# Kernel tuning notes

Hardware: AMD Instinct MI355X
Metric: run time of the kernel (lower is better)

## Reference

```python
import jax, jax.numpy as jnp
import numpy as np

TWO_PI = 2.0 * np.pi
HID, FREQ, OUT = 64, 10, 16
BS, T, K, D = 1024, 128, 8, 32
IN_DIM = K * D


def hard_sigmoid(x):
    # torch.nn.Hardsigmoid: clip(x/6 + 1/2, 0, 1)
    return jnp.clip(x / 6.0 + 0.5, 0.0, 1.0)


def setup_inputs() -> dict:
    key = jax.random.key(0)
    ks = jax.random.split(key, 16)
    s_in = 1.0 / np.sqrt(IN_DIM)
    s_h = 1.0 / np.sqrt(HID)
    inp = {
        "g1": jax.random.normal(ks[0], (BS, T, K, D), jnp.float32),
        "W_i": jax.random.normal(ks[1], (IN_DIM, HID), jnp.float32) * s_in,
        "U_i": jax.random.normal(ks[2], (HID, HID), jnp.float32) * s_h,
        "b_i": jnp.zeros((HID,), jnp.float32),
        "W_ste": jax.random.normal(ks[3], (IN_DIM, HID), jnp.float32) * s_in,
        "U_ste": jax.random.normal(ks[4], (HID, HID), jnp.float32) * s_h,
        "b_ste": jnp.ones((HID,), jnp.float32),
        "W_fre": jax.random.normal(ks[5], (IN_DIM, FREQ), jnp.float32) * s_in,
        "U_fre": jax.random.normal(ks[6], (HID, FREQ), jnp.float32) * s_h,
        "b_fre": jnp.ones((FREQ,), jnp.float32),
        "W_c": jax.random.normal(ks[7], (IN_DIM, HID), jnp.float32) * s_in,
        "U_c": jax.random.normal(ks[8], (HID, HID), jnp.float32) * s_h,
        "b_c": jnp.zeros((HID,), jnp.float32),
        "W_o": jax.random.normal(ks[9], (IN_DIM, HID), jnp.float32) * s_in,
        "U_o": jax.random.normal(ks[10], (HID, HID), jnp.float32) * s_h,
        "b_o": jnp.zeros((HID,), jnp.float32),
        "U_a": jax.random.normal(ks[11], (FREQ, 1), jnp.float32) / np.sqrt(FREQ),
        "b_a": jnp.zeros((HID,), jnp.float32),
        "W_p": jax.random.normal(ks[12], (HID, OUT), jnp.float32) * s_h,
        "b_p": jnp.zeros((OUT,), jnp.float32),
        "fc_w": jax.random.normal(ks[13], (OUT, 1), jnp.float32) / np.sqrt(OUT),
        "fc_b": jnp.zeros((1,), jnp.float32),
    }
    return inp


def reference(g1, W_i, U_i, b_i, W_ste, U_ste, b_ste, W_fre, U_fre, b_fre,
              W_c, U_c, b_c, W_o, U_o, b_o, U_a, b_a, W_p, b_p, fc_w, fc_b):
    bs, Tn, k, d = g1.shape
    x_seq = g1.reshape(bs, Tn, k * d).transpose(1, 0, 2)  # (T, bs, IN)
    H, F = U_i.shape[0], U_fre.shape[1]
    freq = jnp.arange(F, dtype=g1.dtype) / F                 # frequency vector
    h0 = jnp.zeros((bs, H), g1.dtype)
    S0 = jnp.zeros((bs, H, F), g1.dtype)
    times = jnp.arange(1, Tn + 1, dtype=g1.dtype)            # time = t+1 per step

    def step(carry, inp):
        h, S_re, S_im = carry
        x, t = inp
        i = hard_sigmoid(x @ W_i + b_i + h @ U_i)
        ste = hard_sigmoid(x @ W_ste + b_ste + h @ U_ste)    # (bs,H)
        fre = hard_sigmoid(x @ W_fre + b_fre + h @ U_fre)    # (bs,F)
        f = ste[:, :, None] * fre[:, None, :]                # (bs,H,F)
        c = i * jnp.tanh(x @ W_c + b_c + h @ U_c)            # (bs,H)
        omega = TWO_PI * t * freq                            # (F,)
        S_re = f * S_re + c[:, :, None] * jnp.cos(omega)
        S_im = f * S_im + c[:, :, None] * jnp.sin(omega)
        A = S_re * S_re + S_im * S_im                        # (bs,H,F)
        a = jnp.tanh(jnp.einsum('bhf,f->bh', A, U_a[:, 0]) + b_a)
        o = hard_sigmoid(x @ W_o + b_o + h @ U_o)
        return (o * a, S_re, S_im), None

    (hT, _, _), _ = jax.lax.scan(step, (h0, S0, S0), (x_seq, times))
    p = hT @ W_p + b_p                                       # (bs, OUT)
    return p @ fc_w + fc_b                                   # pred: (bs, 1)
```

## Files before the change

kernel.cpp:

```cpp
#include <hip/hip_runtime.h>
#include <cstdint>

#define TSTEPS  128
#define INDIM   256
#define HIDDEN  64
#define FREQN   10
#define NOUT    16
#define XSTRIDE 272
#define NTILE   17

typedef __attribute__((ext_vector_type(8))) short bf16x8;
typedef __attribute__((ext_vector_type(4))) float f32x4;

__device__ __forceinline__ unsigned short bf16h(float x) {
    unsigned u = __float_as_uint(x);
    return (unsigned short)((u + 0x7FFFu + ((u >> 16) & 1u)) >> 16);
}
__device__ __forceinline__ float rdlane(float v, int l) {
    return __int_as_float(__builtin_amdgcn_readlane(__float_as_int(v), l));
}
__device__ __forceinline__ float hsig(float x) {
    return fminf(fmaxf(__fmaf_rn(x, (1.0f / 6.0f), 0.5f), 0.0f), 1.0f);
}
__device__ __forceinline__ float tanh_f(float x) {
    float e = __expf(2.0f * x);
    return 1.0f - 2.0f / (e + 1.0f);
}

__global__ void pack_w(const float* __restrict__ Wi, const float* __restrict__ Wst,
                       const float* __restrict__ Wc, const float* __restrict__ Wo,
                       const float* __restrict__ Wfr,
                       const float* __restrict__ bi, const float* __restrict__ bst,
                       const float* __restrict__ bc, const float* __restrict__ bo,
                       const float* __restrict__ bfr,
                       unsigned short* __restrict__ Wpk, float* __restrict__ bias)
{
    int idx = blockIdx.x * 256 + threadIdx.x;
    if (idx < 8 * NTILE * 64) {
        int l = idx & 63;
        int t = (idx >> 6) % NTILE;
        int s = idx / (64 * NTILE);
        int n = t * 16 + (l & 15);
        unsigned short* dst = Wpk + (size_t)idx * 16;
        #pragma unroll
        for (int i = 0; i < 8; ++i) {
            int k = s * 32 + (l >> 4) * 8 + i;
            float v;
            if      (n < 64)  v = Wi [k * 64 + n];
            else if (n < 128) v = Wst[k * 64 + (n - 64)];
            else if (n < 192) v = Wc [k * 64 + (n - 128)];
            else if (n < 256) v = Wo [k * 64 + (n - 192)];
            else if (n < 266) v = Wfr[k * 10 + (n - 256)];
            else              v = 0.f;
            unsigned short h = bf16h(v);
            float hf = __uint_as_float((unsigned)h << 16);
            dst[i]     = h;
            dst[8 + i] = bf16h(v - hf);
        }
    } else if (idx < 8 * NTILE * 64 + XSTRIDE) {
        int n = idx - 8 * NTILE * 64;
        float b;
        if      (n < 64)  b = bi [n];
        else if (n < 128) b = bst[n - 64];
        else if (n < 192) b = bc [n - 128];
        else if (n < 256) b = bo [n - 192];
        else if (n < 266) b = bfr[n - 256];
        else              b = 0.f;
        bias[n] = b;
    }
}

__global__ __launch_bounds__(256, 2)
void gemm_mfma(const float* __restrict__ A, const unsigned short* __restrict__ Wpk,
               const float* __restrict__ bias, float* __restrict__ outp,
               int ci, int tclog)
{
    const int tid = threadIdx.x;
    const int w   = tid >> 6, l = tid & 63;
    const int l15 = l & 15,  lg = l >> 4;
    const int tcm = (1 << tclog) - 1;
    const int rbase = blockIdx.x * 128 + w * 32;

    f32x4 acc[2][NTILE];
    #pragma unroll
    for (int rt = 0; rt < 2; ++rt)
        #pragma unroll
        for (int t = 0; t < NTILE; ++t) acc[rt][t] = (f32x4){0.f, 0.f, 0.f, 0.f};

    #pragma unroll
    for (int s = 0; s < 8; ++s) {
        bf16x8 ahi[2], alo[2];
        #pragma unroll
        for (int rt = 0; rt < 2; ++rt) {
            int rp   = rbase + rt * 16 + l15;
            int grow = ((rp >> tclog) << 7) + (ci << tclog) + (rp & tcm);
            const float* ap = A + (size_t)grow * INDIM + s * 32 + lg * 8;
            float4 a0 = *reinterpret_cast<const float4*>(ap);
            float4 a1 = *reinterpret_cast<const float4*>(ap + 4);
            float av[8] = {a0.x, a0.y, a0.z, a0.w, a1.x, a1.y, a1.z, a1.w};
            union { bf16x8 v; unsigned short u[8]; } H, L;
            #pragma unroll
            for (int i = 0; i < 8; ++i) {
                unsigned short h = bf16h(av[i]);
                H.u[i] = h;
                L.u[i] = bf16h(av[i] - __uint_as_float((unsigned)h << 16));
            }
            ahi[rt] = H.v; alo[rt] = L.v;
        }
        #pragma unroll
        for (int t = 0; t < NTILE; ++t) {
            const bf16x8* bp =
                reinterpret_cast<const bf16x8*>(Wpk + ((size_t)(s * NTILE + t) * 64 + l) * 16);
            bf16x8 bhi = bp[0], blo = bp[1];
            #pragma unroll
            for (int rt = 0; rt < 2; ++rt) {
                acc[rt][t] = __builtin_amdgcn_mfma_f32_16x16x32_bf16(ahi[rt], bhi, acc[rt][t], 0, 0, 0);
                acc[rt][t] = __builtin_amdgcn_mfma_f32_16x16x32_bf16(ahi[rt], blo, acc[rt][t], 0, 0, 0);
                acc[rt][t] = __builtin_amdgcn_mfma_f32_16x16x32_bf16(alo[rt], bhi, acc[rt][t], 0, 0, 0);
            }
        }
    }
    #pragma unroll
    for (int t = 0; t < NTILE; ++t) {
        float bv = bias[t * 16 + l15];
        #pragma unroll
        for (int rt = 0; rt < 2; ++rt) {
            int rp0 = rbase + rt * 16 + lg * 4;
            #pragma unroll
            for (int r = 0; r < 4; ++r)
                outp[(size_t)(rp0 + r) * XSTRIDE + t * 16 + l15] = acc[rt][t][r] + bv;
        }
    }
}

__global__ void cstab_kernel(float2* __restrict__ tab)
{
    int idx = blockIdx.x * 256 + threadIdx.x;
    if (idx >= TSTEPS * FREQN) return;
    int t = idx / FREQN, j = idx - t * FREQN;
    float time = (float)(t + 1);
    float om = (6.28318530717958647692f * time) * ((float)j / 10.0f);
    float s, c;
    sincosf(om, &s, &c);
    tab[idx] = make_float2(c, s);
}

__global__ __launch_bounds__(256, 3)
void rec_kernel(const float* __restrict__ xproj,
                const float* __restrict__ Ui, const float* __restrict__ Us,
                const float* __restrict__ Uc, const float* __restrict__ Uo,
                const float* __restrict__ Ufre, const float* __restrict__ Ua,
                const float* __restrict__ ba,
                const float2* __restrict__ csTab,
                float* __restrict__ state,
                const float* __restrict__ Wp, const float* __restrict__ bp,
                const float* __restrict__ fcw, const float* __restrict__ fcb,
                float* __restrict__ outv,
                int ci, int TC, int nchunks)
{
    __shared__ f32x4 pg[4][64];
    __shared__ float pf_[4][16];
    __shared__ float hlds[64];
    const int tid  = threadIdx.x;
    const int lane = tid & 63, w = tid >> 6;
    const int row  = blockIdx.x;
    const int k0   = w * 16;
    const int jc   = (lane < FREQN) ? lane : (FREQN - 1);

    float4 Ur[16]; float Uf[16];
    #pragma unroll
    for (int i = 0; i < 16; ++i) {
        int k = k0 + i;
        Ur[i] = make_float4(Ui[k * 64 + lane], Us[k * 64 + lane],
                            Uc[k * 64 + lane], Uo[k * 64 + lane]);
        Uf[i] = Ufre[k * FREQN + jc];
    }

    float hv;
    float Sre[FREQN], Sim[FREQN];
    if (ci == 0) {
        hv = 0.f;
        #pragma unroll
        for (int j = 0; j < FREQN; ++j) { Sre[j] = 0.f; Sim[j] = 0.f; }
    } else {
        hv = state[row * 64 + lane];
        if (w == 0) {
            #pragma unroll
            for (int j = 0; j < FREQN; ++j) {
                Sre[j] = state[65536 + j * 65536 + row * 64 + lane];
                Sim[j] = state[65536 + 655360 + j * 65536 + row * 64 + lane];
            }
        }
    }

    const float ba_l = ba[lane];
    float sua[FREQN];
    #pragma unroll
    for (int j = 0; j < FREQN; ++j) sua[j] = Ua[j];

    const float* xb = xproj + (size_t)row * TC * XSTRIDE;
    float xi = 0.f, xs = 0.f, xc = 0.f, xo = 0.f, xf = 0.f;
    float2 cv = make_float2(0.f, 0.f);
    if (w == 0) {
        xi = xb[lane]; xs = xb[64 + lane]; xc = xb[128 + lane];
        xo = xb[192 + lane]; xf = xb[256 + jc];
        cv = csTab[(ci * TC) * FREQN + jc];
    }

    for (int tt = 0; tt < TC; ++tt) {
        float ai = 0.f, as_ = 0.f, ac = 0.f, ao = 0.f, af = 0.f;
        #pragma unroll
        for (int i = 0; i < 16; ++i) {
            float hk = rdlane(hv, k0 + i);
            ai  = __fmaf_rn(hk, Ur[i].x, ai);
            as_ = __fmaf_rn(hk, Ur[i].y, as_);
            ac  = __fmaf_rn(hk, Ur[i].z, ac);
            ao  = __fmaf_rn(hk, Ur[i].w, ao);
            af  = __fmaf_rn(hk, Uf[i],  af);
        }
        pg[w][lane] = (f32x4){ai, as_, ac, ao};
        if (lane < FREQN) pf_[w][lane] = af;
        __syncthreads();

        if (w == 0) {
            f32x4 q0 = pg[0][lane], q1 = pg[1][lane], q2 = pg[2][lane], q3 = pg[3][lane];
            float si = (q0[0] + q1[0]) + (q2[0] + q3[0]);
            float ss = (q0[1] + q1[1]) + (q2[1] + q3[1]);
            float sc = (q0[2] + q1[2]) + (q2[2] + q3[2]);
            float so = (q0[3] + q1[3]) + (q2[3] + q3[3]);
            float pfr = (pf_[0][jc] + pf_[1][jc]) + (pf_[2][jc] + pf_[3][jc]);
            float cxi = xi, cxs = xs, cxc = xc, cxo = xo, cxf = xf;
            float2 ccv = cv;
            if (tt + 1 < TC) {
                const float* b2 = xb + (size_t)(tt + 1) * XSTRIDE;
                xi = b2[lane]; xs = b2[64 + lane]; xc = b2[128 + lane];
                xo = b2[192 + lane]; xf = b2[256 + jc];
                cv = csTab[(ci * TC + tt + 1) * FREQN + jc];
            }
            float gi = hsig(cxi + si);
            float gs = hsig(cxs + ss);
            float go = hsig(cxo + so);
            float gc = gi * tanh_f(cxc + sc);
            float pfull = cxf + pfr;
            float aacc = 0.f;
            #pragma unroll
            for (int j = 0; j < FREQN; ++j) {
                float fre = hsig(rdlane(pfull, j));
                float cj = rdlane(ccv.x, j);
                float sj = rdlane(ccv.y, j);
                float fj = gs * fre;
                Sre[j] = __fmaf_rn(fj, Sre[j], gc * cj);
                Sim[j] = __fmaf_rn(fj, Sim[j], gc * sj);
                float Aj = __fmaf_rn(Sre[j], Sre[j], Sim[j] * Sim[j]);
                aacc = __fmaf_rn(Aj, sua[j], aacc);
            }
            hlds[lane] = go * tanh_f(aacc + ba_l);
        }
        __syncthreads();
        hv = hlds[lane];
    }

    if (ci == nchunks - 1) {
        if (w == 0) {
            float wef = 0.f;
            #pragma unroll
            for (int o = 0; o < NOUT; ++o)
                wef = __fmaf_rn(Wp[lane * NOUT + o], fcw[o], wef);
            float v = hv * wef;
            #pragma unroll
            for (int off = 32; off > 0; off >>= 1) v += __shfl_xor(v, off, 64);
            if (lane == 0) {
                float cb = fcb[0];
                #pragma unroll
                for (int o = 0; o < NOUT; ++o) cb = __fmaf_rn(bp[o], fcw[o], cb);
                outv[row] = v + cb;
            }
        }
    } else if (w == 0) {
        state[row * 64 + lane] = hv;
        #pragma unroll
        for (int j = 0; j < FREQN; ++j) {
            state[65536 + j * 65536 + row * 64 + lane] = Sre[j];
            state[65536 + 655360 + j * 65536 + row * 64 + lane] = Sim[j];
        }
    }
}

extern "C" void kernel_launch(void* const* d_in, const int* in_sizes, int n_in,
                              void* d_out, int out_size, void* d_ws, size_t ws_size,
                              hipStream_t stream)
{
    const float* g1  = (const float*)d_in[0];
    const float* Wi  = (const float*)d_in[1];
    const float* Ui  = (const float*)d_in[2];
    const float* bi  = (const float*)d_in[3];
    const float* Wst = (const float*)d_in[4];
    const float* Ust = (const float*)d_in[5];
    const float* bst = (const float*)d_in[6];
    const float* Wfr = (const float*)d_in[7];
    const float* Ufq = (const float*)d_in[8];
    const float* bfr = (const float*)d_in[9];
    const float* Wc  = (const float*)d_in[10];
    const float* Uc  = (const float*)d_in[11];
    const float* bc  = (const float*)d_in[12];
    const float* Wo  = (const float*)d_in[13];
    const float* Uo  = (const float*)d_in[14];
    const float* bo  = (const float*)d_in[15];
    const float* Ua  = (const float*)d_in[16];
    const float* ba  = (const float*)d_in[17];
    const float* Wp  = (const float*)d_in[18];
    const float* bp  = (const float*)d_in[19];
    const float* fcw = (const float*)d_in[20];
    const float* fcb = (const float*)d_in[21];
    float* outv = (float*)d_out;

    const size_t stateFloats = 65536 + 2 * 655360;
    const size_t csFloats    = TSTEPS * FREQN * 2;
    const size_t wpkShorts   = (size_t)8 * NTILE * 64 * 16;
    int TC = 128;
    while (TC > 8 &&
           ((size_t)1024 * TC * XSTRIDE + stateFloats + csFloats + XSTRIDE) * 4
               + wpkShorts * 2 > ws_size)
        TC >>= 1;
    int tclog = 31 - __builtin_clz((unsigned)TC);
    int nchunks = TSTEPS / TC;

    float*  xproj = (float*)d_ws;
    float*  state = xproj + (size_t)1024 * TC * XSTRIDE;
    float2* csTab = (float2*)(state + stateFloats);
    float*  bias  = (float*)(csTab + TSTEPS * FREQN);
    unsigned short* Wpk = (unsigned short*)(bias + XSTRIDE);

    pack_w<<<36, 256, 0, stream>>>(Wi, Wst, Wc, Wo, Wfr, bi, bst, bc, bo, bfr, Wpk, bias);
    cstab_kernel<<<(TSTEPS * FREQN + 255) / 256, 256, 0, stream>>>(csTab);

    const int Mt = (1024 * TC) / 128;
    for (int ci = 0; ci < nchunks; ++ci) {
        gemm_mfma<<<Mt, 256, 0, stream>>>(g1, Wpk, bias, xproj, ci, tclog);
        rec_kernel<<<1024, 256, 0, stream>>>(xproj, Ui, Ust, Uc, Uo, Ufq, Ua, ba,
                                             csTab, state, Wp, bp, fcw, fcb, outv,
                                             ci, TC, nchunks);
    }
}
```

Before: 554.1 us.

## Process two batch rows per 512-thread block in the recurrent kernel

The recurrent kernel now launches 512-thread blocks, each handling two batch rows, so 512 blocks run instead of 1024. Each of the 8 waves keeps 8 rows of the U matrices in registers and computes partial products for both rows, and two waves then run the gate and state update in parallel instead of one. The sin/cos table is read as scalar loads rather than broadcast with readlane, and hard-sigmoid on the frequency gate is applied before the broadcast. The aim is to spread the serial per-step work across more waves and reuse the U registers for two rows, at the cost of larger reductions through shared memory and fewer blocks.

```diff
diff --git a/kernel.cpp b/kernel.cpp
--- a/kernel.cpp
+++ b/kernel.cpp
@@ -145,50 +145,52 @@
     tab[idx] = make_float2(c, s);
 }
 
-__global__ __launch_bounds__(256, 3)
+__global__ __launch_bounds__(512, 2)
 void rec_kernel(const float* __restrict__ xproj,
                 const float* __restrict__ Ui, const float* __restrict__ Us,
                 const float* __restrict__ Uc, const float* __restrict__ Uo,
                 const float* __restrict__ Ufre, const float* __restrict__ Ua,
                 const float* __restrict__ ba,
-                const float2* __restrict__ csTab,
+                const float* __restrict__ csTab,
                 float* __restrict__ state,
                 const float* __restrict__ Wp, const float* __restrict__ bp,
                 const float* __restrict__ fcw, const float* __restrict__ fcb,
                 float* __restrict__ outv,
                 int ci, int TC, int nchunks)
 {
-    __shared__ f32x4 pg[4][64];
-    __shared__ float pf_[4][16];
-    __shared__ float hlds[64];
+    __shared__ f32x4 pg[2][8][64];
+    __shared__ float pf_[2][8][16];
+    __shared__ float hlds[2][64];
     const int tid  = threadIdx.x;
     const int lane = tid & 63, w = tid >> 6;
-    const int row  = blockIdx.x;
-    const int k0   = w * 16;
+    const int row0 = blockIdx.x * 2;
+    const int myrow = row0 + w;
+    const int k0   = w * 8;
     const int jc   = (lane < FREQN) ? lane : (FREQN - 1);
 
-    float4 Ur[16]; float Uf[16];
-    #pragma unroll
-    for (int i = 0; i < 16; ++i) {
+    float4 Ur[8]; float Uf[8];
+    #pragma unroll
+    for (int i = 0; i < 8; ++i) {
         int k = k0 + i;
         Ur[i] = make_float4(Ui[k * 64 + lane], Us[k * 64 + lane],
                             Uc[k * 64 + lane], Uo[k * 64 + lane]);
         Uf[i] = Ufre[k * FREQN + jc];
     }
 
-    float hv;
+    float hv0, hv1;
     float Sre[FREQN], Sim[FREQN];
     if (ci == 0) {
-        hv = 0.f;
+        hv0 = 0.f; hv1 = 0.f;
         #pragma unroll
         for (int j = 0; j < FREQN; ++j) { Sre[j] = 0.f; Sim[j] = 0.f; }
     } else {
-        hv = state[row * 64 + lane];
-        if (w == 0) {
+        hv0 = state[row0 * 64 + lane];
+        hv1 = state[(row0 + 1) * 64 + lane];
+        if (w < 2) {
             #pragma unroll
             for (int j = 0; j < FREQN; ++j) {
-                Sre[j] = state[65536 + j * 65536 + row * 64 + lane];
-                Sim[j] = state[65536 + 655360 + j * 65536 + row * 64 + lane];
+                Sre[j] = state[65536 + j * 65536 + myrow * 64 + lane];
+                Sim[j] = state[65536 + 655360 + j * 65536 + myrow * 64 + lane];
             }
         }
     }
@@ -198,90 +200,94 @@
     #pragma unroll
     for (int j = 0; j < FREQN; ++j) sua[j] = Ua[j];
 
-    const float* xb = xproj + (size_t)row * TC * XSTRIDE;
+    const float* xb = xproj + (size_t)myrow * TC * XSTRIDE;
     float xi = 0.f, xs = 0.f, xc = 0.f, xo = 0.f, xf = 0.f;
-    float2 cv = make_float2(0.f, 0.f);
-    if (w == 0) {
+    if (w < 2) {
         xi = xb[lane]; xs = xb[64 + lane]; xc = xb[128 + lane];
         xo = xb[192 + lane]; xf = xb[256 + jc];
-        cv = csTab[(ci * TC) * FREQN + jc];
     }
 
     for (int tt = 0; tt < TC; ++tt) {
-        float ai = 0.f, as_ = 0.f, ac = 0.f, ao = 0.f, af = 0.f;
-        #pragma unroll
-        for (int i = 0; i < 16; ++i) {
-            float hk = rdlane(hv, k0 + i);
-            ai  = __fmaf_rn(hk, Ur[i].x, ai);
-            as_ = __fmaf_rn(hk, Ur[i].y, as_);
-            ac  = __fmaf_rn(hk, Ur[i].z, ac);
-            ao  = __fmaf_rn(hk, Ur[i].w, ao);
-            af  = __fmaf_rn(hk, Uf[i],  af);
-        }
-        pg[w][lane] = (f32x4){ai, as_, ac, ao};
-        if (lane < FREQN) pf_[w][lane] = af;
+        float a0i = 0.f, a0s = 0.f, a0c = 0.f, a0o = 0.f, a0f = 0.f;
+        float a1i = 0.f, a1s = 0.f, a1c = 0.f, a1o = 0.f, a1f = 0.f;
+        #pragma unroll
+        for (int i = 0; i < 8; ++i) {
+            float h0 = rdlane(hv0, k0 + i);
+            float h1 = rdlane(hv1, k0 + i);
+            a0i = __fmaf_rn(h0, Ur[i].x, a0i);  a1i = __fmaf_rn(h1, Ur[i].x, a1i);
+            a0s = __fmaf_rn(h0, Ur[i].y, a0s);  a1s = __fmaf_rn(h1, Ur[i].y, a1s);
+            a0c = __fmaf_rn(h0, Ur[i].z, a0c);  a1c = __fmaf_rn(h1, Ur[i].z, a1c);
+            a0o = __fmaf_rn(h0, Ur[i].w, a0o);  a1o = __fmaf_rn(h1, Ur[i].w, a1o);
+            a0f = __fmaf_rn(h0, Uf[i],  a0f);   a1f = __fmaf_rn(h1, Uf[i],  a1f);
+        }
+        pg[0][w][lane] = (f32x4){a0i, a0s, a0c, a0o};
+        pg[1][w][lane] = (f32x4){a1i, a1s, a1c, a1o};
+        if (lane < 16) { pf_[0][w][lane] = a0f; pf_[1][w][lane] = a1f; }
         __syncthreads();
 
-        if (w == 0) {
-            f32x4 q0 = pg[0][lane], q1 = pg[1][lane], q2 = pg[2][lane], q3 = pg[3][lane];
-            float si = (q0[0] + q1[0]) + (q2[0] + q3[0]);
-            float ss = (q0[1] + q1[1]) + (q2[1] + q3[1]);
-            float sc = (q0[2] + q1[2]) + (q2[2] + q3[2]);
-            float so = (q0[3] + q1[3]) + (q2[3] + q3[3]);
-            float pfr = (pf_[0][jc] + pf_[1][jc]) + (pf_[2][jc] + pf_[3][jc]);
+        if (w < 2) {
+            f32x4 q0 = pg[w][0][lane], q1 = pg[w][1][lane];
+            f32x4 q2 = pg[w][2][lane], q3 = pg[w][3][lane];
+            f32x4 q4 = pg[w][4][lane], q5 = pg[w][5][lane];
+            f32x4 q6 = pg[w][6][lane], q7 = pg[w][7][lane];
+            f32x4 qs = ((q0 + q1) + (q2 + q3)) + ((q4 + q5) + (q6 + q7));
+            float pfr = ((pf_[w][0][jc] + pf_[w][1][jc]) + (pf_[w][2][jc] + pf_[w][3][jc]))
+                      + ((pf_[w][4][jc] + pf_[w][5][jc]) + (pf_[w][6][jc] + pf_[w][7][jc]));
             float cxi = xi, cxs = xs, cxc = xc, cxo = xo, cxf = xf;
-            float2 ccv = cv;
             if (tt + 1 < TC) {
                 const float* b2 = xb + (size_t)(tt + 1) * XSTRIDE;
                 xi = b2[lane]; xs = b2[64 + lane]; xc = b2[128 + lane];
                 xo = b2[192 + lane]; xf = b2[256 + jc];
-                cv = csTab[(ci * TC + tt + 1) * FREQN + jc];
-            }
-            float gi = hsig(cxi + si);
-            float gs = hsig(cxs + ss);
-            float go = hsig(cxo + so);
-            float gc = gi * tanh_f(cxc + sc);
-            float pfull = cxf + pfr;
+            }
+            const float* cs = csTab + (size_t)(ci * TC + tt) * (2 * FREQN);
+            float gi = hsig(cxi + qs[0]);
+            float gs = hsig(cxs + qs[1]);
+            float go = hsig(cxo + qs[3]);
+            float gc = gi * tanh_f(cxc + qs[2]);
+            float freh = hsig(cxf + pfr);
             float aacc = 0.f;
             #pragma unroll
             for (int j = 0; j < FREQN; ++j) {
-                float fre = hsig(rdlane(pfull, j));
-                float cj = rdlane(ccv.x, j);
-                float sj = rdlane(ccv.y, j);
+                float fre = rdlane(freh, j);
+                float cj = cs[2 * j];
+                float sj = cs[2 * j + 1];
                 float fj = gs * fre;
                 Sre[j] = __fmaf_rn(fj, Sre[j], gc * cj);
                 Sim[j] = __fmaf_rn(fj, Sim[j], gc * sj);
                 float Aj = __fmaf_rn(Sre[j], Sre[j], Sim[j] * Sim[j]);
                 aacc = __fmaf_rn(Aj, sua[j], aacc);
             }
-            hlds[lane] = go * tanh_f(aacc + ba_l);
+            hlds[w][lane] = go * tanh_f(aacc + ba_l);
         }
         __syncthreads();
-        hv = hlds[lane];
+        hv0 = hlds[0][lane];
+        hv1 = hlds[1][lane];
     }
 
     if (ci == nchunks - 1) {
-        if (w == 0) {
+        if (w < 2) {
+            float hvm = (w == 0) ? hv0 : hv1;
             float wef = 0.f;
             #pragma unroll
             for (int o = 0; o < NOUT; ++o)
                 wef = __fmaf_rn(Wp[lane * NOUT + o], fcw[o], wef);
-            float v = hv * wef;
+            float v = hvm * wef;
             #pragma unroll
             for (int off = 32; off > 0; off >>= 1) v += __shfl_xor(v, off, 64);
             if (lane == 0) {
                 float cb = fcb[0];
                 #pragma unroll
                 for (int o = 0; o < NOUT; ++o) cb = __fmaf_rn(bp[o], fcw[o], cb);
-                outv[row] = v + cb;
-            }
-        }
-    } else if (w == 0) {
-        state[row * 64 + lane] = hv;
+                outv[myrow] = v + cb;
+            }
+        }
+    } else if (w < 2) {
+        float hvm = (w == 0) ? hv0 : hv1;
+        state[myrow * 64 + lane] = hvm;
         #pragma unroll
         for (int j = 0; j < FREQN; ++j) {
-            state[65536 + j * 65536 + row * 64 + lane] = Sre[j];
-            state[65536 + 655360 + j * 65536 + row * 64 + lane] = Sim[j];
+            state[65536 + j * 65536 + myrow * 64 + lane] = Sre[j];
+            state[65536 + 655360 + j * 65536 + myrow * 64 + lane] = Sim[j];
         }
     }
 }
@@ -327,18 +333,18 @@
 
     float*  xproj = (float*)d_ws;
     float*  state = xproj + (size_t)1024 * TC * XSTRIDE;
-    float2* csTab = (float2*)(state + stateFloats);
-    float*  bias  = (float*)(csTab + TSTEPS * FREQN);
+    float*  csTab = state + stateFloats;
+    float*  bias  = csTab + csFloats;
     unsigned short* Wpk = (unsigned short*)(bias + XSTRIDE);
 
     pack_w<<<36, 256, 0, stream>>>(Wi, Wst, Wc, Wo, Wfr, bi, bst, bc, bo, bfr, Wpk, bias);
-    cstab_kernel<<<(TSTEPS * FREQN + 255) / 256, 256, 0, stream>>>(csTab);
+    cstab_kernel<<<(TSTEPS * FREQN + 255) / 256, 256, 0, stream>>>((float2*)csTab);
 
     const int Mt = (1024 * TC) / 128;
     for (int ci = 0; ci < nchunks; ++ci) {
         gemm_mfma<<<Mt, 256, 0, stream>>>(g1, Wpk, bias, xproj, ci, tclog);
-        rec_kernel<<<1024, 256, 0, stream>>>(xproj, Ui, Ust, Uc, Uo, Ufq, Ua, ba,
-                                             csTab, state, Wp, bp, fcw, fcb, outv,
-                                             ci, TC, nchunks);
-    }
-}
+        rec_kernel<<<512, 512, 0, stream>>>(xproj, Ui, Ust, Uc, Uo, Ufq, Ua, ba,
+                                            csTab, state, Wp, bp, fcw, fcb, outv,
+                                            ci, TC, nchunks);
+    }
+}
```

New measurement: 613.9 us. +10.8%, slower.

## Run one batch row per wavefront with fp16 dot2 recurrent matvec

Applied to the files above, without the earlier changes.

The recurrent kernel changes from four waves cooperating on one batch row, with LDS reductions and two block barriers per step, to one wave owning a whole row, four rows per block. All 64x(4*64+10) recurrent weights are kept in registers as packed fp16 pairs, and the hidden state is broadcast through a per-wave LDS buffer of fp16 pairs consumed by v_dot2 instructions. The change removes the cross-wave reductions and block syncs and lets every wave do useful gate and state work instead of only wave 0. In exchange it uses many more registers (occupancy bound dropped to 1), launches a quarter as many blocks, and introduces fp16 rounding of weights and hidden state, which may affect accuracy.

```diff
diff --git a/kernel.cpp b/kernel.cpp
--- a/kernel.cpp
+++ b/kernel.cpp
@@ -11,6 +11,8 @@
 
 typedef __attribute__((ext_vector_type(8))) short bf16x8;
 typedef __attribute__((ext_vector_type(4))) float f32x4;
+typedef _Float16 f16;
+typedef __attribute__((ext_vector_type(2))) _Float16 f16x2;
 
 __device__ __forceinline__ unsigned short bf16h(float x) {
     unsigned u = __float_as_uint(x);
@@ -25,6 +27,13 @@
 __device__ __forceinline__ float tanh_f(float x) {
     float e = __expf(2.0f * x);
     return 1.0f - 2.0f / (e + 1.0f);
+}
+__device__ __forceinline__ float fdot2(f16x2 a, f16x2 b, float c) {
+#if __has_builtin(__builtin_amdgcn_fdot2)
+    return __builtin_amdgcn_fdot2(a, b, c, false);
+#else
+    return __fmaf_rn((float)a.x, (float)b.x, __fmaf_rn((float)a.y, (float)b.y, c));
+#endif
 }
 
 __global__ void pack_w(const float* __restrict__ Wi, const float* __restrict__ Wst,
@@ -145,35 +154,35 @@
     tab[idx] = make_float2(c, s);
 }
 
-__global__ __launch_bounds__(256, 3)
+__global__ __launch_bounds__(256, 1)
 void rec_kernel(const float* __restrict__ xproj,
                 const float* __restrict__ Ui, const float* __restrict__ Us,
                 const float* __restrict__ Uc, const float* __restrict__ Uo,
                 const float* __restrict__ Ufre, const float* __restrict__ Ua,
                 const float* __restrict__ ba,
-                const float2* __restrict__ csTab,
+                const float* __restrict__ csTab,
                 float* __restrict__ state,
                 const float* __restrict__ Wp, const float* __restrict__ bp,
                 const float* __restrict__ fcw, const float* __restrict__ fcb,
                 float* __restrict__ outv,
                 int ci, int TC, int nchunks)
 {
-    __shared__ f32x4 pg[4][64];
-    __shared__ float pf_[4][16];
-    __shared__ float hlds[64];
+    __shared__ __align__(16) unsigned hx[4][32];
     const int tid  = threadIdx.x;
     const int lane = tid & 63, w = tid >> 6;
-    const int row  = blockIdx.x;
-    const int k0   = w * 16;
+    const int row  = blockIdx.x * 4 + w;
     const int jc   = (lane < FREQN) ? lane : (FREQN - 1);
 
-    float4 Ur[16]; float Uf[16];
-    #pragma unroll
-    for (int i = 0; i < 16; ++i) {
-        int k = k0 + i;
-        Ur[i] = make_float4(Ui[k * 64 + lane], Us[k * 64 + lane],
-                            Uc[k * 64 + lane], Uo[k * 64 + lane]);
-        Uf[i] = Ufre[k * FREQN + jc];
+    f16x2 Uk[32][4];
+    f16x2 Uf2[32];
+    #pragma unroll
+    for (int m = 0; m < 32; ++m) {
+        int ka = 2 * m, kb = 2 * m + 1;
+        Uk[m][0] = (f16x2){(f16)Ui[ka * 64 + lane], (f16)Ui[kb * 64 + lane]};
+        Uk[m][1] = (f16x2){(f16)Us[ka * 64 + lane], (f16)Us[kb * 64 + lane]};
+        Uk[m][2] = (f16x2){(f16)Uc[ka * 64 + lane], (f16)Uc[kb * 64 + lane]};
+        Uk[m][3] = (f16x2){(f16)Uo[ka * 64 + lane], (f16)Uo[kb * 64 + lane]};
+        Uf2[m]   = (f16x2){(f16)Ufre[ka * FREQN + jc], (f16)Ufre[kb * FREQN + jc]};
     }
 
     float hv;
@@ -184,12 +193,10 @@
         for (int j = 0; j < FREQN; ++j) { Sre[j] = 0.f; Sim[j] = 0.f; }
     } else {
         hv = state[row * 64 + lane];
-        if (w == 0) {
-            #pragma unroll
-            for (int j = 0; j < FREQN; ++j) {
-                Sre[j] = state[65536 + j * 65536 + row * 64 + lane];
-                Sim[j] = state[65536 + 655360 + j * 65536 + row * 64 + lane];
-            }
+        #pragma unroll
+        for (int j = 0; j < FREQN; ++j) {
+            Sre[j] = state[65536 + j * 65536 + row * 64 + lane];
+            Sim[j] = state[65536 + 655360 + j * 65536 + row * 64 + lane];
         }
     }
 
@@ -198,85 +205,79 @@
     #pragma unroll
     for (int j = 0; j < FREQN; ++j) sua[j] = Ua[j];
 
+    {
+        float hb = __shfl_down(hv, 1, 64);
+        f16x2 hp; hp.x = (f16)hv; hp.y = (f16)hb;
+        if (!(lane & 1)) hx[w][lane >> 1] = __builtin_bit_cast(unsigned, hp);
+    }
+
     const float* xb = xproj + (size_t)row * TC * XSTRIDE;
-    float xi = 0.f, xs = 0.f, xc = 0.f, xo = 0.f, xf = 0.f;
-    float2 cv = make_float2(0.f, 0.f);
-    if (w == 0) {
-        xi = xb[lane]; xs = xb[64 + lane]; xc = xb[128 + lane];
-        xo = xb[192 + lane]; xf = xb[256 + jc];
-        cv = csTab[(ci * TC) * FREQN + jc];
-    }
+    float xi = xb[lane], xs = xb[64 + lane], xc = xb[128 + lane];
+    float xo = xb[192 + lane], xf = xb[256 + jc];
 
     for (int tt = 0; tt < TC; ++tt) {
+        unsigned hw_[32];
+        #pragma unroll
+        for (int m = 0; m < 32; ++m) hw_[m] = hx[w][m];
+
         float ai = 0.f, as_ = 0.f, ac = 0.f, ao = 0.f, af = 0.f;
         #pragma unroll
-        for (int i = 0; i < 16; ++i) {
-            float hk = rdlane(hv, k0 + i);
-            ai  = __fmaf_rn(hk, Ur[i].x, ai);
-            as_ = __fmaf_rn(hk, Ur[i].y, as_);
-            ac  = __fmaf_rn(hk, Ur[i].z, ac);
-            ao  = __fmaf_rn(hk, Ur[i].w, ao);
-            af  = __fmaf_rn(hk, Uf[i],  af);
-        }
-        pg[w][lane] = (f32x4){ai, as_, ac, ao};
-        if (lane < FREQN) pf_[w][lane] = af;
-        __syncthreads();
-
-        if (w == 0) {
-            f32x4 q0 = pg[0][lane], q1 = pg[1][lane], q2 = pg[2][lane], q3 = pg[3][lane];
-            float si = (q0[0] + q1[0]) + (q2[0] + q3[0]);
-            float ss = (q0[1] + q1[1]) + (q2[1] + q3[1]);
-            float sc = (q0[2] + q1[2]) + (q2[2] + q3[2]);
-            float so = (q0[3] + q1[3]) + (q2[3] + q3[3]);
-            float pfr = (pf_[0][jc] + pf_[1][jc]) + (pf_[2][jc] + pf_[3][jc]);
-            float cxi = xi, cxs = xs, cxc = xc, cxo = xo, cxf = xf;
-            float2 ccv = cv;
-            if (tt + 1 < TC) {
-                const float* b2 = xb + (size_t)(tt + 1) * XSTRIDE;
-                xi = b2[lane]; xs = b2[64 + lane]; xc = b2[128 + lane];
-                xo = b2[192 + lane]; xf = b2[256 + jc];
-                cv = csTab[(ci * TC + tt + 1) * FREQN + jc];
-            }
-            float gi = hsig(cxi + si);
-            float gs = hsig(cxs + ss);
-            float go = hsig(cxo + so);
-            float gc = gi * tanh_f(cxc + sc);
-            float pfull = cxf + pfr;
-            float aacc = 0.f;
+        for (int m = 0; m < 32; ++m) {
+            f16x2 h2 = __builtin_bit_cast(f16x2, hw_[m]);
+            ai  = fdot2(h2, Uk[m][0], ai);
+            as_ = fdot2(h2, Uk[m][1], as_);
+            ac  = fdot2(h2, Uk[m][2], ac);
+            ao  = fdot2(h2, Uk[m][3], ao);
+            af  = fdot2(h2, Uf2[m],  af);
+        }
+
+        float cxi = xi, cxs = xs, cxc = xc, cxo = xo, cxf = xf;
+        if (tt + 1 < TC) {
+            const float* b2 = xb + (size_t)(tt + 1) * XSTRIDE;
+            xi = b2[lane]; xs = b2[64 + lane]; xc = b2[128 + lane];
+            xo = b2[192 + lane]; xf = b2[256 + jc];
+        }
+        const float* cs = csTab + (size_t)(ci * TC + tt) * (2 * FREQN);
+
+        float gi = hsig(cxi + ai);
+        float gs = hsig(cxs + as_);
+        float go = hsig(cxo + ao);
+        float gc = gi * tanh_f(cxc + ac);
+        float freh = hsig(cxf + af);
+        float aacc = 0.f;
+        #pragma unroll
+        for (int j = 0; j < FREQN; ++j) {
+            float fre = rdlane(freh, j);
+            float cj = cs[2 * j];
+            float sj = cs[2 * j + 1];
+            float fj = gs * fre;
+            Sre[j] = __fmaf_rn(fj, Sre[j], gc * cj);
+            Sim[j] = __fmaf_rn(fj, Sim[j], gc * sj);
+            float Aj = __fmaf_rn(Sre[j], Sre[j], Sim[j] * Sim[j]);
+            aacc = __fmaf_rn(Aj, sua[j], aacc);
+        }
+        hv = go * tanh_f(aacc + ba_l);
+
+        float hb = __shfl_down(hv, 1, 64);
+        f16x2 hp; hp.x = (f16)hv; hp.y = (f16)hb;
+        if (!(lane & 1)) hx[w][lane >> 1] = __builtin_bit_cast(unsigned, hp);
+    }
+
+    if (ci == nchunks - 1) {
+        float wef = 0.f;
+        #pragma unroll
+        for (int o = 0; o < NOUT; ++o)
+            wef = __fmaf_rn(Wp[lane * NOUT + o], fcw[o], wef);
+        float v = hv * wef;
+        #pragma unroll
+        for (int off = 32; off > 0; off >>= 1) v += __shfl_xor(v, off, 64);
+        if (lane == 0) {
+            float cb = fcb[0];
             #pragma unroll
-            for (int j = 0; j < FREQN; ++j) {
-                float fre = hsig(rdlane(pfull, j));
-                float cj = rdlane(ccv.x, j);
-                float sj = rdlane(ccv.y, j);
-                float fj = gs * fre;
-                Sre[j] = __fmaf_rn(fj, Sre[j], gc * cj);
-                Sim[j] = __fmaf_rn(fj, Sim[j], gc * sj);
-                float Aj = __fmaf_rn(Sre[j], Sre[j], Sim[j] * Sim[j]);
-                aacc = __fmaf_rn(Aj, sua[j], aacc);
-            }
-            hlds[lane] = go * tanh_f(aacc + ba_l);
-        }
-        __syncthreads();
-        hv = hlds[lane];
-    }
-
-    if (ci == nchunks - 1) {
-        if (w == 0) {
-            float wef = 0.f;
-            #pragma unroll
-            for (int o = 0; o < NOUT; ++o)
-                wef = __fmaf_rn(Wp[lane * NOUT + o], fcw[o], wef);
-            float v = hv * wef;
-            #pragma unroll
-            for (int off = 32; off > 0; off >>= 1) v += __shfl_xor(v, off, 64);
-            if (lane == 0) {
-                float cb = fcb[0];
-                #pragma unroll
-                for (int o = 0; o < NOUT; ++o) cb = __fmaf_rn(bp[o], fcw[o], cb);
-                outv[row] = v + cb;
-            }
-        }
-    } else if (w == 0) {
+            for (int o = 0; o < NOUT; ++o) cb = __fmaf_rn(bp[o], fcw[o], cb);
+            outv[row] = v + cb;
+        }
+    } else {
         state[row * 64 + lane] = hv;
         #pragma unroll
         for (int j = 0; j < FREQN; ++j) {
@@ -327,18 +328,18 @@
 
     float*  xproj = (float*)d_ws;
     float*  state = xproj + (size_t)1024 * TC * XSTRIDE;
-    float2* csTab = (float2*)(state + stateFloats);
-    float*  bias  = (float*)(csTab + TSTEPS * FREQN);
+    float*  csTab = state + stateFloats;
+    float*  bias  = csTab + csFloats;
     unsigned short* Wpk = (unsigned short*)(bias + XSTRIDE);
 
     pack_w<<<36, 256, 0, stream>>>(Wi, Wst, Wc, Wo, Wfr, bi, bst, bc, bo, bfr, Wpk, bias);
-    cstab_kernel<<<(TSTEPS * FREQN + 255) / 256, 256, 0, stream>>>(csTab);
+    cstab_kernel<<<(TSTEPS * FREQN + 255) / 256, 256, 0, stream>>>((float2*)csTab);
 
     const int Mt = (1024 * TC) / 128;
     for (int ci = 0; ci < nchunks; ++ci) {
         gemm_mfma<<<Mt, 256, 0, stream>>>(g1, Wpk, bias, xproj, ci, tclog);
-        rec_kernel<<<1024, 256, 0, stream>>>(xproj, Ui, Ust, Uc, Uo, Ufq, Ua, ba,
-                                             csTab, state, Wp, bp, fcw, fcb, outv,
-                                             ci, TC, nchunks);
-    }
-}
+        rec_kernel<<<256, 256, 0, stream>>>(xproj, Ui, Ust, Uc, Uo, Ufq, Ua, ba,
+                                            csTab, state, Wp, bp, fcw, fcb, outv,
+                                            ci, TC, nchunks);
+    }
+}
```

New measurement: 479.0 us. -13.6%, faster.
